# Optimization experiments

Measured on AMD Instinct MI355X. Metric: run time of the kernel, lower is better.

## Reference

```python
import jax, jax.numpy as jnp
import numpy as np

NUM_CODES = 8192
CODE_DIM = 64
DECAY = 0.99
EPS = 1e-05


def setup_inputs() -> dict:
    key = jax.random.key(0)
    k1, k2 = jax.random.split(key)
    z = jax.random.normal(k1, (8, CODE_DIM, 64, 64), dtype=jnp.float32)
    embed = jax.random.normal(k2, (NUM_CODES, CODE_DIM), dtype=jnp.float32)
    embed = embed / jnp.linalg.norm(embed, axis=1, keepdims=True)  # F.normalize(dim=1)
    cluster_size = jnp.zeros((NUM_CODES,), dtype=jnp.float32)
    embed_avg = embed * 1.0
    return {"z": z, "embed": embed, "cluster_size": cluster_size, "embed_avg": embed_avg}


def reference(z, embed, cluster_size, embed_avg):
    B, C, H, W = z.shape
    # (B,C,H,W) -> (N, C), N = B*H*W
    flat = jnp.transpose(z, (0, 2, 3, 1)).reshape(-1, C)
    x2 = jnp.sum(flat * flat, axis=1, keepdims=True)
    e2 = jnp.sum(embed * embed, axis=1)[None, :]
    logits = x2 + e2 - 2.0 * (flat @ embed.T)
    codes = jnp.argmin(logits, axis=1)
    # gather nearest code vectors, restore (B,C,H,W)
    z_q = jnp.transpose(embed[codes].reshape(B, H, W, C), (0, 3, 1, 2))
    # EMA update (training path; equivalent to one-hot matmul via segment sums)
    cs_batch = jax.ops.segment_sum(jnp.ones_like(codes, dtype=flat.dtype), codes, num_segments=NUM_CODES)
    embed_sum = jax.ops.segment_sum(flat, codes, num_segments=NUM_CODES)
    new_cluster_size = cluster_size * DECAY + cs_batch * (1.0 - DECAY)
    new_embed_avg = embed_avg * DECAY + embed_sum * (1.0 - DECAY)
    n = jnp.sum(new_cluster_size)
    cs_smoothed = (new_cluster_size + EPS) / (n + NUM_CODES * EPS) * n
    new_embed = new_embed_avg / cs_smoothed[:, None]
    new_embed = new_embed / jnp.linalg.norm(new_embed, axis=1, keepdims=True)
    return z_q, codes.reshape(B, H, W), new_embed, new_cluster_size, new_embed_avg
```

## Files before the change

kernel.cpp:

```cpp
#include <hip/hip_runtime.h>
#include <math.h>
#include <float.h>

#define NPTS   32768
#define NCODES 8192
#define D      64
#define HWSZ   4096
#define KSPLIT 8
#define NSTAGE 8

#define DECAY_F 0.99f
#define OMD_F   ((float)(1.0 - 0.99))
#define EPS_F   1e-5f

typedef __attribute__((ext_vector_type(8)))  short bf16x8;
typedef __attribute__((ext_vector_type(8)))  unsigned short us8;
typedef __attribute__((ext_vector_type(4)))  float f32x4;
typedef __attribute__((ext_vector_type(16))) float f32x16;

#define ZQ_OFF    0
#define CODES_OFF 2097152
#define NE_OFF    2129920
#define NCS_OFF   2654208
#define NEA_OFF   2662400

#define WS_PSUM   0
#define WS_ME2    64
#define WS_HIST   8256
#define WS_BOFF   16448
#define WS_BOFF2  24640
#define WS_CODES  32832
#define WS_ORDER  65600
#define WS_PMG    98368
#define WS_EBI    1146944
#define WS_ZROW   1409088

__device__ __forceinline__ unsigned short f2bf(float x) {
    unsigned int u = __float_as_uint(x);
    unsigned int r = (u + 0x7fffu + ((u >> 16) & 1u)) >> 16;
    return (unsigned short)r;
}
__device__ __forceinline__ float bf2f(unsigned short b) {
    return __uint_as_float(((unsigned int)b) << 16);
}

__global__ __launch_bounds__(256) void k_prep_e(
    const float* __restrict__ embed,
    unsigned short* __restrict__ ebi,
    float* __restrict__ me2, int* __restrict__ hist)
{
    const int tid = threadIdx.x;
    const int c = blockIdx.x * 32 + (tid >> 3);
    const int s = tid & 7;
    const float4 v0 = *(const float4*)(embed + (size_t)c * D + s * 8);
    const float4 v1 = *(const float4*)(embed + (size_t)c * D + s * 8 + 4);
    float x[8] = {v0.x, v0.y, v0.z, v0.w, v1.x, v1.y, v1.z, v1.w};
    float s2 = 0.f;
#pragma unroll
    for (int j = 0; j < 8; ++j) s2 += x[j] * x[j];
    s2 += __shfl_xor(s2, 1);
    s2 += __shfl_xor(s2, 2);
    s2 += __shfl_xor(s2, 4);
    us8 p0, p1;
#pragma unroll
    for (int j = 0; j < 8; ++j) {
        unsigned short a = f2bf(x[j]);
        float r = x[j] - bf2f(a);
        p0[j] = a; p1[j] = f2bf(r);
    }
    const int sg = c >> 7, ci = c & 127;
    unsigned short* tile = ebi + (size_t)sg * 16384;
    *(us8*)(tile + s * 1024 + ci * 8) = p0;
    *(us8*)(tile + 8192 + s * 1024 + ci * 8) = p1;
    if (s == 0) {
        me2[c] = -0.5f * s2;
        hist[c] = 0;
    }
}

#define MFMA32 __builtin_amdgcn_mfma_f32_32x32x16_bf16

#define TOP2(nt, g, gi) { \
    bool c1 = (g) > b1m[nt]; \
    bool c2 = (g) > b2m[nt]; \
    b2m[nt] = c1 ? b1m[nt] : (c2 ? (g) : b2m[nt]); \
    b2g[nt] = c1 ? b1g[nt] : (c2 ? (gi) : b2g[nt]); \
    b1m[nt] = c1 ? (g) : b1m[nt]; \
    b1g[nt] = c1 ? (gi) : b1g[nt]; }

#define GMAX8(a, o) fmaxf(fmaxf(fmaxf(fmaxf(a[o+0], a[o+1]), a[o+2]), \
                                fmaxf(fmaxf(a[o+3], a[o+4]), a[o+5])), \
                          fmaxf(a[o+6], a[o+7]))

__global__ __launch_bounds__(256, 2) void k_argmin_mfma(
    const float* __restrict__ z,
    const unsigned short* __restrict__ ebi,
    float* __restrict__ pmg)
{
    __shared__ __align__(16) char ets[2 * 32768];

    const int tid = threadIdx.x;
    const int l = tid & 63;
    const int w = tid >> 6;
    const int l31 = l & 31;
    const int hi = l >> 5;
    const int split = blockIdx.x >> 7;
    const int pgrp  = blockIdx.x & 127;
    const int n0    = pgrp * 256;
    const int b     = n0 >> 12;
    const int hw0   = n0 & 4095;
    const int ptw   = n0 + w * 64;

    const char* ebase = (const char*)ebi;
#define ISSUE_STAGE(sg_, buf_) { \
    const char* gsrc_ = ebase + (size_t)(sg_) * 32768; \
    _Pragma("unroll") \
    for (int i_ = 0; i_ < 8; ++i_) { \
        __builtin_amdgcn_global_load_lds( \
            (const __attribute__((address_space(1))) void*)(gsrc_ + i_ * 4096 + w * 1024 + l * 16), \
            (__attribute__((address_space(3))) void*)(ets + (buf_) * 32768 + i_ * 4096 + w * 1024), \
            16, 0, 0); \
    } }

    ISSUE_STAGE(split * NSTAGE, 0)

    const float* zb = z + (size_t)b * D * HWSZ;
    us8 zf[2][2][4];
#pragma unroll
    for (int nt = 0; nt < 2; ++nt) {
        const int hwp = hw0 + w * 64 + nt * 32 + l31;
#pragma unroll
        for (int kc = 0; kc < 4; ++kc) {
            us8 p0, p1;
#pragma unroll
            for (int j = 0; j < 8; ++j) {
                float x = zb[(size_t)(kc * 16 + hi * 8 + j) * HWSZ + hwp];
                unsigned short a = f2bf(x);
                float r = x - bf2f(a);
                p0[j] = a; p1[j] = f2bf(r);
            }
            zf[nt][0][kc] = p0; zf[nt][1][kc] = p1;
        }
    }

    f32x16 zerov;
#pragma unroll
    for (int r = 0; r < 16; ++r) zerov[r] = 0.f;

    __syncthreads();

    float b1m[2] = {-FLT_MAX, -FLT_MAX}, b2m[2] = {-FLT_MAX, -FLT_MAX};
    int   b1g[2] = {0, 0},               b2g[2] = {0, 0};

    for (int stg = 0; stg < NSTAGE; ++stg) {
        const int sg = split * NSTAGE + stg;
        if (stg + 1 < NSTAGE) ISSUE_STAGE(sg + 1, (stg + 1) & 1)

        const char* bt = ets + (stg & 1) * 32768;
#pragma unroll
        for (int ct = 0; ct < 4; ++ct) {
            f32x16 acc0, acc1;
#pragma unroll
            for (int kc = 0; kc < 4; ++kc) {
                const size_t off = (size_t)(kc * 2 + hi) * 2048 + (size_t)(ct * 32 + l31) * 16;
                bf16x8 ea0 = *(const bf16x8*)(bt + off);
                bf16x8 ea1 = *(const bf16x8*)(bt + 16384 + off);
                if (kc == 0) {
                    acc0 = MFMA32(ea1, (bf16x8)zf[0][0][0], zerov, 0, 0, 0);
                    acc1 = MFMA32(ea1, (bf16x8)zf[1][0][0], zerov, 0, 0, 0);
                } else {
                    acc0 = MFMA32(ea1, (bf16x8)zf[0][0][kc], acc0, 0, 0, 0);
                    acc1 = MFMA32(ea1, (bf16x8)zf[1][0][kc], acc1, 0, 0, 0);
                }
                acc0 = MFMA32(ea0, (bf16x8)zf[0][1][kc], acc0, 0, 0, 0);
                acc1 = MFMA32(ea0, (bf16x8)zf[1][1][kc], acc1, 0, 0, 0);
                acc0 = MFMA32(ea0, (bf16x8)zf[0][0][kc], acc0, 0, 0, 0);
                acc1 = MFMA32(ea0, (bf16x8)zf[1][0][kc], acc1, 0, 0, 0);
            }

            const int gb = sg * 16 + ct * 4 + hi;
            {
                float g00 = GMAX8(acc0, 0);
                float g01 = GMAX8(acc0, 8);
                float g10 = GMAX8(acc1, 0);
                float g11 = GMAX8(acc1, 8);
                TOP2(0, g00, gb)
                TOP2(0, g01, gb + 2)
                TOP2(1, g10, gb)
                TOP2(1, g11, gb + 2)
            }
        }
        __syncthreads();
    }

#pragma unroll
    for (int nt = 0; nt < 2; ++nt) {
        float o1 = __shfl_xor(b1m[nt], 32); int o1g = __shfl_xor(b1g[nt], 32);
        float o2 = __shfl_xor(b2m[nt], 32); int o2g = __shfl_xor(b2g[nt], 32);
        float n1m, n2m; int n1g, n2g;
        if (o1 > b1m[nt]) {
            n1m = o1; n1g = o1g;
            if (b1m[nt] >= o2) { n2m = b1m[nt]; n2g = b1g[nt]; } else { n2m = o2; n2g = o2g; }
        } else {
            n1m = b1m[nt]; n1g = b1g[nt];
            if (o1 >= b2m[nt]) { n2m = o1; n2g = o1g; } else { n2m = b2m[nt]; n2g = b2g[nt]; }
        }
        b1m[nt] = n1m; b1g[nt] = n1g; b2m[nt] = n2m; b2g[nt] = n2g;
    }
    if (l < 32) {
#pragma unroll
        for (int nt = 0; nt < 2; ++nt) {
            int pt = ptw + nt * 32 + l31;
            float4 v = {b1m[nt], __int_as_float(b1g[nt]), b2m[nt], __int_as_float(b2g[nt])};
            *(float4*)(pmg + ((size_t)split * NPTS + pt) * 4) = v;
        }
    }
}

__device__ __forceinline__ int grp_code(int g, int s) {
    int base = (g >> 4) * 128 + ((g >> 2) & 3) * 32 + ((g >> 1) & 1) * 16 + (g & 1) * 4;
    return base + (s & 3) + ((s >> 2) & 1) * 8;
}

__global__ __launch_bounds__(256) void k_refine(
    const float* __restrict__ z, const float* __restrict__ embed,
    const float* __restrict__ me2, const float* __restrict__ pmg,
    int* __restrict__ codes_i, float* __restrict__ out_codes,
    float* __restrict__ zq, int* __restrict__ hist, float* __restrict__ zrow)
{
    __shared__ float  xs[64 * 32];
    __shared__ float4 smg[256];
    __shared__ float  sbm[256];
    __shared__ int    sbi[256];
    const int tid = threadIdx.x;
    const int pi = tid & 31, s = tid >> 5;
    const int n0 = blockIdx.x * 32;
    const int b = n0 >> 12, hw0 = n0 & 4095;
    const int n = n0 + pi;

    {
        float4 v = ((const float4*)pmg)[(size_t)(tid & 7) * NPTS + n0 + (tid >> 3)];
        smg[(tid & 7) * 32 + (tid >> 3)] = v;
    }
    const float* zb = z + (size_t)b * D * HWSZ + hw0;
#pragma unroll
    for (int i = 0; i < 8; ++i) {
        int c = s * 8 + i;
        xs[c * 32 + pi] = zb[(size_t)c * HWSZ + pi];
    }
    __syncthreads();
    float x[64];
#pragma unroll
    for (int c = 0; c < 64; ++c) x[c] = xs[c * 32 + pi];

    float t1 = -FLT_MAX, t2 = -FLT_MAX; int g1 = 0, g2 = 0;
#pragma unroll
    for (int j = 0; j < 8; ++j) {
        float4 v = smg[j * 32 + pi];
        float m1 = v.x; int a1 = __float_as_int(v.y);
        float m2 = v.z; int a2 = __float_as_int(v.w);
        if (m1 > t1) { t2 = t1; g2 = g1; t1 = m1; g1 = a1; }
        else if (m1 > t2) { t2 = m1; g2 = a1; }
        if (m2 > t1) { t2 = t1; g2 = g1; t1 = m2; g1 = a2; }
        else if (m2 > t2) { t2 = m2; g2 = a2; }
    }

    float bm = -FLT_MAX; int bi = 0x7fffffff;
#pragma unroll
    for (int cset = 0; cset < 2; ++cset) {
        const int ci = grp_code(cset ? g2 : g1, s);
        const float4* er = (const float4*)(embed + (size_t)ci * D);
        float d0 = 0.f, d1 = 0.f, d2 = 0.f, d3 = 0.f;
#pragma unroll
        for (int q = 0; q < 16; ++q) {
            float4 e4 = er[q];
            d0 = fmaf(x[4 * q + 0], e4.x, d0);
            d1 = fmaf(x[4 * q + 1], e4.y, d1);
            d2 = fmaf(x[4 * q + 2], e4.z, d2);
            d3 = fmaf(x[4 * q + 3], e4.w, d3);
        }
        float m = ((d0 + d1) + (d2 + d3)) + me2[ci];
        if (m > bm || (m == bm && ci < bi)) { bm = m; bi = ci; }
    }
    sbm[tid] = bm; sbi[tid] = bi;
    __syncthreads();

    if (s == 0) {
        float B = sbm[pi]; int I = sbi[pi];
#pragma unroll
        for (int t = 1; t < 8; ++t) {
            float mm = sbm[t * 32 + pi]; int ii = sbi[t * 32 + pi];
            if (mm > B || (mm == B && ii < I)) { B = mm; I = ii; }
        }
        codes_i[n] = I;
        out_codes[n] = (float)I;
        atomicAdd(&hist[I], 1);
        const float* err = embed + (size_t)I * D;
        size_t zoff = (size_t)b * D * HWSZ + hw0 + pi;
#pragma unroll 8
        for (int c = 0; c < 64; ++c) zq[zoff + (size_t)c * HWSZ] = err[c];
    }
    {
        float4 a4 = {x[s * 8 + 0], x[s * 8 + 1], x[s * 8 + 2], x[s * 8 + 3]};
        float4 b4 = {x[s * 8 + 4], x[s * 8 + 5], x[s * 8 + 6], x[s * 8 + 7]};
        *(float4*)(zrow + (size_t)n * 64 + s * 8) = a4;
        *(float4*)(zrow + (size_t)n * 64 + s * 8 + 4) = b4;
    }
}

__global__ __launch_bounds__(1024) void k_scan(
    const int* __restrict__ hist, const float* __restrict__ cs_in,
    int* __restrict__ binoff, int* __restrict__ binoff2, float* __restrict__ psum)
{
    __shared__ int wtot[16];
    __shared__ int wbase[16];
    __shared__ float csw[16];
    const int tid = threadIdx.x;
    const int lane = tid & 63, w = tid >> 6;
    int v[8]; int s = 0;
    float cz = 0.f;
#pragma unroll
    for (int i = 0; i < 8; ++i) {
        v[i] = hist[tid * 8 + i];
        s += v[i];
        cz += cs_in[tid * 8 + i];
    }
    int inc = s;
#pragma unroll
    for (int off = 1; off < 64; off <<= 1) {
        int t = __shfl_up(inc, off);
        if (lane >= off) inc += t;
    }
    cz += __shfl_xor(cz, 32); cz += __shfl_xor(cz, 16); cz += __shfl_xor(cz, 8);
    cz += __shfl_xor(cz, 4);  cz += __shfl_xor(cz, 2);  cz += __shfl_xor(cz, 1);
    if (lane == 63) wtot[w] = inc;
    if (lane == 0)  csw[w] = cz;
    __syncthreads();
    if (tid == 0) {
        int a = 0;
        float S = 0.f;
#pragma unroll
        for (int i = 0; i < 16; ++i) { int t = wtot[i]; wbase[i] = a; a += t; S += csw[i]; }
        psum[0] = S;
    }
    __syncthreads();
    int excl = wbase[w] + (inc - s);
#pragma unroll
    for (int i = 0; i < 8; ++i) {
        binoff[tid * 8 + i] = excl;
        binoff2[tid * 8 + i] = excl;
        excl += v[i];
    }
}

__global__ void k_reorder(const int* __restrict__ codes_i,
                          int* __restrict__ binoff2, int* __restrict__ order)
{
    int n = blockIdx.x * 256 + threadIdx.x;
    int c = codes_i[n];
    int r = atomicAdd(&binoff2[c], 1);
    order[r] = n;
}

__global__ __launch_bounds__(256) void k_accum(
    const int* __restrict__ hist, const int* __restrict__ binoff,
    const int* __restrict__ order, const float* __restrict__ zrow,
    const float* __restrict__ cs, const float* __restrict__ eavg,
    const float* __restrict__ psum,
    float* __restrict__ out_ncs, float* __restrict__ out_nea, float* __restrict__ out_ne)
{
    int k = blockIdx.x * 4 + (threadIdx.x >> 6);
    int lane = threadIdx.x & 63;
    int cnt = hist[k], base = binoff[k];
    float acc = 0.f;
    for (int i = 0; i < cnt; ++i) {
        int p = order[base + i];
        acc += zrow[(size_t)p * 64 + lane];
    }
    float S = psum[0];
    float n = DECAY_F * S + OMD_F * (float)NPTS;

    float v = cs[k] * DECAY_F + (float)cnt * OMD_F;
    if (lane == 0) out_ncs[k] = v;

    int idx = k * D + lane;
    float ea = eavg[idx] * DECAY_F + acc * OMD_F;
    out_nea[idx] = ea;
    float csm = (v + EPS_F) / (n + (float)NCODES * EPS_F) * n;
    float u = ea / csm;
    float ss = u * u;
    ss += __shfl_xor(ss, 32);
    ss += __shfl_xor(ss, 16);
    ss += __shfl_xor(ss, 8);
    ss += __shfl_xor(ss, 4);
    ss += __shfl_xor(ss, 2);
    ss += __shfl_xor(ss, 1);
    out_ne[idx] = u / sqrtf(ss);
}

extern "C" void kernel_launch(void* const* d_in, const int* in_sizes, int n_in,
                              void* d_out, int out_size, void* d_ws, size_t ws_size,
                              hipStream_t stream) {
    const float* z     = (const float*)d_in[0];
    const float* embed = (const float*)d_in[1];
    const float* cs    = (const float*)d_in[2];
    const float* eavg  = (const float*)d_in[3];

    float* out = (float*)d_out;
    float* zq        = out + ZQ_OFF;
    float* out_codes = out + CODES_OFF;
    float* out_ne    = out + NE_OFF;
    float* out_ncs   = out + NCS_OFF;
    float* out_nea   = out + NEA_OFF;

    float* ws = (float*)d_ws;
    float* psum   = ws + WS_PSUM;
    float* me2    = ws + WS_ME2;
    int*   hist   = (int*)(ws + WS_HIST);
    int*   boff   = (int*)(ws + WS_BOFF);
    int*   boff2  = (int*)(ws + WS_BOFF2);
    int*   codesi = (int*)(ws + WS_CODES);
    int*   order  = (int*)(ws + WS_ORDER);
    float* pmg    = ws + WS_PMG;
    float* zrow   = ws + WS_ZROW;
    unsigned short* ebi = (unsigned short*)(ws + WS_EBI);

    k_prep_e<<<NCODES / 32, 256, 0, stream>>>(embed, ebi, me2, hist);
    k_argmin_mfma<<<128 * KSPLIT, 256, 0, stream>>>(z, ebi, pmg);
    k_refine<<<NPTS / 32, 256, 0, stream>>>(z, embed, me2, pmg,
                                            codesi, out_codes, zq, hist, zrow);
    k_scan<<<1, 1024, 0, stream>>>(hist, cs, boff, boff2, psum);
    k_reorder<<<NPTS / 256, 256, 0, stream>>>(codesi, boff2, order);
    k_accum<<<NCODES / 4, 256, 0, stream>>>(hist, boff, order, zrow, cs, eavg, psum,
                                            out_ncs, out_nea, out_ne);
}
```

Measured before the change: 136.5 us.

## Give each wave its own code stream with per-wave LDS buffers and no block barriers

The argmin kernel changes from block-wide 128-code stages to per-wave 32-code stages. Each wave streams its own double-buffered LDS slice, synchronised with explicit waitcnts instead of __syncthreads. Each wave now holds 128 points (4 MFMA N-tiles), so every loaded code tile is reused across more points, and the grid is halved. The embed tile layout and grp_code mapping change to match. Separately, the refine kernel spreads the z_q gather-write over all 8 thread groups using vector loads instead of one group writing 64 scalars. The per-wave scheme duplicates code-tile loads across the four waves and raises register pressure from the extra accumulators and z fragments.

```diff
diff --git a/kernel.cpp b/kernel.cpp
--- a/kernel.cpp
+++ b/kernel.cpp
@@ -7,7 +7,7 @@
 #define D      64
 #define HWSZ   4096
 #define KSPLIT 8
-#define NSTAGE 8
+#define NSTAGE 32
 
 #define DECAY_F 0.99f
 #define OMD_F   ((float)(1.0 - 0.99))
@@ -68,10 +68,10 @@
         float r = x[j] - bf2f(a);
         p0[j] = a; p1[j] = f2bf(r);
     }
-    const int sg = c >> 7, ci = c & 127;
-    unsigned short* tile = ebi + (size_t)sg * 16384;
-    *(us8*)(tile + s * 1024 + ci * 8) = p0;
-    *(us8*)(tile + 8192 + s * 1024 + ci * 8) = p1;
+    const int sg = c >> 5, ci = c & 31;
+    unsigned short* tile = ebi + (size_t)sg * 4096;
+    *(us8*)(tile + s * 256 + ci * 8) = p0;
+    *(us8*)(tile + 2048 + s * 256 + ci * 8) = p1;
     if (s == 0) {
         me2[c] = -0.5f * s2;
         hist[c] = 0;
@@ -97,38 +97,41 @@
     const unsigned short* __restrict__ ebi,
     float* __restrict__ pmg)
 {
-    __shared__ __align__(16) char ets[2 * 32768];
+    __shared__ __align__(16) char ets[4 * 16384];
 
     const int tid = threadIdx.x;
     const int l = tid & 63;
     const int w = tid >> 6;
     const int l31 = l & 31;
     const int hi = l >> 5;
-    const int split = blockIdx.x >> 7;
-    const int pgrp  = blockIdx.x & 127;
-    const int n0    = pgrp * 256;
+    const int split = blockIdx.x >> 6;
+    const int pgrp  = blockIdx.x & 63;
+    const int n0    = pgrp * 512;
     const int b     = n0 >> 12;
     const int hw0   = n0 & 4095;
-    const int ptw   = n0 + w * 64;
-
+    const int ptw   = n0 + w * 128;
+
+    char* wbuf = ets + w * 16384;
     const char* ebase = (const char*)ebi;
+
 #define ISSUE_STAGE(sg_, buf_) { \
-    const char* gsrc_ = ebase + (size_t)(sg_) * 32768; \
+    const char* gsrc_ = ebase + (size_t)(sg_) * 8192; \
+    char* ldst_ = wbuf + (buf_) * 8192; \
     _Pragma("unroll") \
     for (int i_ = 0; i_ < 8; ++i_) { \
         __builtin_amdgcn_global_load_lds( \
-            (const __attribute__((address_space(1))) void*)(gsrc_ + i_ * 4096 + w * 1024 + l * 16), \
-            (__attribute__((address_space(3))) void*)(ets + (buf_) * 32768 + i_ * 4096 + w * 1024), \
+            (const __attribute__((address_space(1))) void*)(gsrc_ + i_ * 1024 + l * 16), \
+            (__attribute__((address_space(3))) void*)(ldst_ + i_ * 1024), \
             16, 0, 0); \
     } }
 
     ISSUE_STAGE(split * NSTAGE, 0)
 
     const float* zb = z + (size_t)b * D * HWSZ;
-    us8 zf[2][2][4];
-#pragma unroll
-    for (int nt = 0; nt < 2; ++nt) {
-        const int hwp = hw0 + w * 64 + nt * 32 + l31;
+    us8 zf[4][2][4];
+#pragma unroll
+    for (int nt = 0; nt < 4; ++nt) {
+        const int hwp = hw0 + w * 128 + nt * 32 + l31;
 #pragma unroll
         for (int kc = 0; kc < 4; ++kc) {
             us8 p0, p1;
@@ -147,54 +150,74 @@
 #pragma unroll
     for (int r = 0; r < 16; ++r) zerov[r] = 0.f;
 
-    __syncthreads();
-
-    float b1m[2] = {-FLT_MAX, -FLT_MAX}, b2m[2] = {-FLT_MAX, -FLT_MAX};
-    int   b1g[2] = {0, 0},               b2g[2] = {0, 0};
+    float b1m[4], b2m[4]; int b1g[4], b2g[4];
+#pragma unroll
+    for (int nt = 0; nt < 4; ++nt) {
+        b1m[nt] = -FLT_MAX; b2m[nt] = -FLT_MAX; b1g[nt] = 0; b2g[nt] = 0;
+    }
 
     for (int stg = 0; stg < NSTAGE; ++stg) {
         const int sg = split * NSTAGE + stg;
-        if (stg + 1 < NSTAGE) ISSUE_STAGE(sg + 1, (stg + 1) & 1)
-
-        const char* bt = ets + (stg & 1) * 32768;
-#pragma unroll
-        for (int ct = 0; ct < 4; ++ct) {
-            f32x16 acc0, acc1;
-#pragma unroll
-            for (int kc = 0; kc < 4; ++kc) {
-                const size_t off = (size_t)(kc * 2 + hi) * 2048 + (size_t)(ct * 32 + l31) * 16;
-                bf16x8 ea0 = *(const bf16x8*)(bt + off);
-                bf16x8 ea1 = *(const bf16x8*)(bt + 16384 + off);
-                if (kc == 0) {
-                    acc0 = MFMA32(ea1, (bf16x8)zf[0][0][0], zerov, 0, 0, 0);
-                    acc1 = MFMA32(ea1, (bf16x8)zf[1][0][0], zerov, 0, 0, 0);
-                } else {
-                    acc0 = MFMA32(ea1, (bf16x8)zf[0][0][kc], acc0, 0, 0, 0);
-                    acc1 = MFMA32(ea1, (bf16x8)zf[1][0][kc], acc1, 0, 0, 0);
-                }
-                acc0 = MFMA32(ea0, (bf16x8)zf[0][1][kc], acc0, 0, 0, 0);
-                acc1 = MFMA32(ea0, (bf16x8)zf[1][1][kc], acc1, 0, 0, 0);
-                acc0 = MFMA32(ea0, (bf16x8)zf[0][0][kc], acc0, 0, 0, 0);
-                acc1 = MFMA32(ea0, (bf16x8)zf[1][0][kc], acc1, 0, 0, 0);
+        asm volatile("s_waitcnt lgkmcnt(0)" ::: "memory");
+        __builtin_amdgcn_sched_barrier(0);
+        if (stg + 1 < NSTAGE) {
+            ISSUE_STAGE(sg + 1, (stg + 1) & 1)
+            asm volatile("s_waitcnt vmcnt(8)" ::: "memory");
+        } else {
+            asm volatile("s_waitcnt vmcnt(0)" ::: "memory");
+        }
+        __builtin_amdgcn_sched_barrier(0);
+
+        const char* bt = wbuf + (stg & 1) * 8192;
+
+        f32x16 acc0, acc1, acc2, acc3;
+        __builtin_amdgcn_s_setprio(1);
+#pragma unroll
+        for (int kc = 0; kc < 4; ++kc) {
+            const size_t off = (size_t)(kc * 2 + hi) * 512 + (size_t)l31 * 16;
+            bf16x8 ea0 = *(const bf16x8*)(bt + off);
+            bf16x8 ea1 = *(const bf16x8*)(bt + 4096 + off);
+            if (kc == 0) {
+                acc0 = MFMA32(ea1, (bf16x8)zf[0][0][0], zerov, 0, 0, 0);
+                acc1 = MFMA32(ea1, (bf16x8)zf[1][0][0], zerov, 0, 0, 0);
+                acc2 = MFMA32(ea1, (bf16x8)zf[2][0][0], zerov, 0, 0, 0);
+                acc3 = MFMA32(ea1, (bf16x8)zf[3][0][0], zerov, 0, 0, 0);
+            } else {
+                acc0 = MFMA32(ea1, (bf16x8)zf[0][0][kc], acc0, 0, 0, 0);
+                acc1 = MFMA32(ea1, (bf16x8)zf[1][0][kc], acc1, 0, 0, 0);
+                acc2 = MFMA32(ea1, (bf16x8)zf[2][0][kc], acc2, 0, 0, 0);
+                acc3 = MFMA32(ea1, (bf16x8)zf[3][0][kc], acc3, 0, 0, 0);
             }
-
-            const int gb = sg * 16 + ct * 4 + hi;
-            {
-                float g00 = GMAX8(acc0, 0);
-                float g01 = GMAX8(acc0, 8);
-                float g10 = GMAX8(acc1, 0);
-                float g11 = GMAX8(acc1, 8);
-                TOP2(0, g00, gb)
-                TOP2(0, g01, gb + 2)
-                TOP2(1, g10, gb)
-                TOP2(1, g11, gb + 2)
-            }
-        }
-        __syncthreads();
-    }
-
-#pragma unroll
-    for (int nt = 0; nt < 2; ++nt) {
+            acc0 = MFMA32(ea0, (bf16x8)zf[0][1][kc], acc0, 0, 0, 0);
+            acc1 = MFMA32(ea0, (bf16x8)zf[1][1][kc], acc1, 0, 0, 0);
+            acc2 = MFMA32(ea0, (bf16x8)zf[2][1][kc], acc2, 0, 0, 0);
+            acc3 = MFMA32(ea0, (bf16x8)zf[3][1][kc], acc3, 0, 0, 0);
+            acc0 = MFMA32(ea0, (bf16x8)zf[0][0][kc], acc0, 0, 0, 0);
+            acc1 = MFMA32(ea0, (bf16x8)zf[1][0][kc], acc1, 0, 0, 0);
+            acc2 = MFMA32(ea0, (bf16x8)zf[2][0][kc], acc2, 0, 0, 0);
+            acc3 = MFMA32(ea0, (bf16x8)zf[3][0][kc], acc3, 0, 0, 0);
+        }
+        __builtin_amdgcn_s_setprio(0);
+
+        {
+            const int gb = sg * 4 + hi;
+            float g00 = GMAX8(acc0, 0), g01 = GMAX8(acc0, 8);
+            float g10 = GMAX8(acc1, 0), g11 = GMAX8(acc1, 8);
+            float g20 = GMAX8(acc2, 0), g21 = GMAX8(acc2, 8);
+            float g30 = GMAX8(acc3, 0), g31 = GMAX8(acc3, 8);
+            TOP2(0, g00, gb)
+            TOP2(0, g01, gb + 2)
+            TOP2(1, g10, gb)
+            TOP2(1, g11, gb + 2)
+            TOP2(2, g20, gb)
+            TOP2(2, g21, gb + 2)
+            TOP2(3, g30, gb)
+            TOP2(3, g31, gb + 2)
+        }
+    }
+
+#pragma unroll
+    for (int nt = 0; nt < 4; ++nt) {
         float o1 = __shfl_xor(b1m[nt], 32); int o1g = __shfl_xor(b1g[nt], 32);
         float o2 = __shfl_xor(b2m[nt], 32); int o2g = __shfl_xor(b2g[nt], 32);
         float n1m, n2m; int n1g, n2g;
@@ -209,7 +232,7 @@
     }
     if (l < 32) {
 #pragma unroll
-        for (int nt = 0; nt < 2; ++nt) {
+        for (int nt = 0; nt < 4; ++nt) {
             int pt = ptw + nt * 32 + l31;
             float4 v = {b1m[nt], __int_as_float(b1g[nt]), b2m[nt], __int_as_float(b2g[nt])};
             *(float4*)(pmg + ((size_t)split * NPTS + pt) * 4) = v;
@@ -218,7 +241,7 @@
 }
 
 __device__ __forceinline__ int grp_code(int g, int s) {
-    int base = (g >> 4) * 128 + ((g >> 2) & 3) * 32 + ((g >> 1) & 1) * 16 + (g & 1) * 4;
+    int base = (g >> 2) * 32 + ((g >> 1) & 1) * 16 + (g & 1) * 4;
     return base + (s & 3) + ((s >> 2) & 1) * 8;
 }
 
@@ -295,10 +318,19 @@
         codes_i[n] = I;
         out_codes[n] = (float)I;
         atomicAdd(&hist[I], 1);
+        sbi[pi] = I;
+    }
+    __syncthreads();
+    {
+        const int I = sbi[pi];
         const float* err = embed + (size_t)I * D;
+        const float4 e0 = *(const float4*)(err + s * 8);
+        const float4 e1 = *(const float4*)(err + s * 8 + 4);
+        float ev[8] = {e0.x, e0.y, e0.z, e0.w, e1.x, e1.y, e1.z, e1.w};
         size_t zoff = (size_t)b * D * HWSZ + hw0 + pi;
-#pragma unroll 8
-        for (int c = 0; c < 64; ++c) zq[zoff + (size_t)c * HWSZ] = err[c];
+#pragma unroll
+        for (int j = 0; j < 8; ++j)
+            zq[zoff + (size_t)(s * 8 + j) * HWSZ] = ev[j];
     }
     {
         float4 a4 = {x[s * 8 + 0], x[s * 8 + 1], x[s * 8 + 2], x[s * 8 + 3]};
@@ -426,7 +458,7 @@
     unsigned short* ebi = (unsigned short*)(ws + WS_EBI);
 
     k_prep_e<<<NCODES / 32, 256, 0, stream>>>(embed, ebi, me2, hist);
-    k_argmin_mfma<<<128 * KSPLIT, 256, 0, stream>>>(z, ebi, pmg);
+    k_argmin_mfma<<<64 * KSPLIT, 256, 0, stream>>>(z, ebi, pmg);
     k_refine<<<NPTS / 32, 256, 0, stream>>>(z, embed, me2, pmg,
                                             codesi, out_codes, zq, hist, zrow);
     k_scan<<<1, 1024, 0, stream>>>(hist, cs, boff, boff2, psum);
```

After: 145.7 us. 6.8% more time.
